# Optimization experiments

Hardware: AMD Instinct MI355X
Metric: run time of the kernel (lower is better)

Reference implementation:

```python
import jax, jax.numpy as jnp
import numpy as np

N = 50000      # nodes
E = 600000     # edges
A = 8          # max attrs per node
DT = 64        # node type embed dim
DA = 64        # node attr embed dim
C = DT + DA    # annotation dim = GGNN channels
T = 16         # num node types
TE = 4         # num edge types
L = 4          # num_agg_steps
B = 256        # num graphs
VATTR = 1000   # num node attrs
ENC = 128      # encoder_output_dim
NCLS = 10      # decoder output classes


def setup_inputs() -> dict:
    key = jax.random.key(0)
    ks = jax.random.split(key, 16)
    s = 0.05
    x_type = jax.random.randint(ks[0], (N,), 0, T)
    x_attrs = jax.random.randint(ks[1], (N, A), 0, VATTR)
    x_attrs_mask = jax.random.randint(ks[2], (N,), 1, A + 1)  # >=1 valid attr per node
    edge_index = jax.random.randint(ks[3], (2, E), 0, N)
    edge_attr = jax.random.randint(ks[4], (E,), 0, TE)
    batch = jnp.sort(jax.random.randint(ks[5], (N,), 0, B))
    return {
        'x_type': x_type, 'x_attrs': x_attrs, 'x_attrs_mask': x_attrs_mask,
        'edge_index': edge_index, 'edge_attr': edge_attr,
        'num_graphs': int(B), 'batch': batch,
        'type_emb': jax.random.normal(ks[6], (T, DT)) * s,
        'attr_emb': jax.random.normal(ks[7], (VATTR, DA)) * s,
        'W_msg': jax.random.normal(ks[8], (L, TE, C, C)) * s,
        'W_ih': jax.random.normal(ks[9], (3 * C, C)) * s,
        'W_hh': jax.random.normal(ks[10], (3 * C, C)) * s,
        'b_ih': jnp.zeros((3 * C,)),
        'b_hh': jnp.zeros((3 * C,)),
        'w_attn': jax.random.normal(ks[11], (C,)) * s,
        'b_attn': jnp.zeros(()),
        'W_enc': jax.random.normal(ks[12], (T * C, ENC)) * s,
        'b_enc': jnp.zeros((ENC,)),
        'W_dec': jax.random.normal(ks[13], (ENC, NCLS)) * s,
        'b_dec': jnp.zeros((NCLS,)),
    }


def _gru_cell(m, h, W_ih, W_hh, b_ih, b_hh):
    gi = m @ W_ih.T + b_ih            # [N, 3C]
    gh = h @ W_hh.T + b_hh            # [N, 3C]
    ir, iz, inn = jnp.split(gi, 3, axis=-1)
    hr, hz, hn = jnp.split(gh, 3, axis=-1)
    r = jax.nn.sigmoid(ir + hr)
    z = jax.nn.sigmoid(iz + hz)
    n = jnp.tanh(inn + r * hn)
    return (1.0 - z) * n + z * h


def reference(x_type, x_attrs, x_attrs_mask, edge_index, edge_attr, num_graphs, batch,
              type_emb, attr_emb, W_msg, W_ih, W_hh, b_ih, b_hh,
              w_attn, b_attn, W_enc, b_enc, W_dec, b_dec):
    n = x_type.shape[0]
    # --- embed node types and ragged-mean attribute embeddings ---
    t_emb = type_emb[x_type]                                   # [N, DT]
    a_all = attr_emb[x_attrs]                                  # [N, A, DA]
    valid = (jnp.arange(A)[None, :] < x_attrs_mask[:, None]).astype(a_all.dtype)
    a_emb = (a_all * valid[..., None]).sum(1) / jnp.maximum(x_attrs_mask, 1)[:, None].astype(a_all.dtype)
    x = jnp.concatenate([t_emb, a_emb], axis=1)                # [N, C]

    # --- GatedGraphConv with per-edge-type weights (sum aggregation + GRU) ---
    src, dst = edge_index[0], edge_index[1]
    for l in range(L):
        h_all = jnp.einsum('nc,tcd->tnd', x, W_msg[l])         # [TE, N, C]
        m_e = h_all.reshape(TE * n, C)[edge_attr * n + src]    # [E, C] gather per edge
        m = jax.ops.segment_sum(m_e, dst, num_segments=n)      # [N, C]
        x = _gru_cell(m, x, W_ih, W_hh, b_ih, b_hh)

    # --- per-(graph, node_type) segment mean (zeros for empty groups) ---
    seg = batch * T + x_type                                   # [N]
    S = num_graphs * T
    sums = jax.ops.segment_sum(x, seg, num_segments=S)         # [B*T, C]
    cnt = jax.ops.segment_sum(jnp.ones((n,), x.dtype), seg, num_segments=S)
    agg = jnp.where(cnt[:, None] > 0, sums / jnp.maximum(cnt, 1.0)[:, None], 0.0)
    agg = agg.reshape(num_graphs, T, C)                        # [B, T, C]

    # --- attention over node types, flatten, encode, decode ---
    w = agg @ w_attn + b_attn                                  # [B, T]
    attn = jax.nn.softmax(w, axis=-1)
    flat = (attn[..., None] * agg).reshape(num_graphs, T * C)  # [B, T*C]
    enc = flat @ W_enc + b_enc                                 # [B, ENC]
    return enc @ W_dec + b_dec                                 # [B, NCLS]
```

## Files before the change

kernel.cpp:

```cpp
#include <hip/hip_runtime.h>
#include <hip/hip_bf16.h>

#define NN 50000
#define NP 50016
#define EE 600000
#define AA 8
#define CC 128
#define TT 16
#define TE 4
#define LL 4
#define BB 256
#define ENC 128
#define NCLS 10
#define SROW 136
#define STR 520

typedef __attribute__((ext_vector_type(8))) short bf16x8;
typedef __attribute__((ext_vector_type(4))) float fx4;

__device__ __forceinline__ float b2f(ushort u) {
    union { float f; uint32_t i; } v; v.i = ((uint32_t)u) << 16; return v.f;
}
__device__ __forceinline__ ushort f2b(float f) {
    union { float f; uint32_t i; } v; v.f = f;
    uint32_t x = v.i;
    x += 0x7FFFu + ((x >> 16) & 1u);
    return (ushort)(x >> 16);
}
__device__ __forceinline__ float ldw(const void* p, long i, int isf) {
    return isf ? ((const float*)p)[i] : b2f(((const ushort*)p)[i]);
}
__device__ __forceinline__ float sigm(float t) { return 1.f / (1.f + __expf(-t)); }

__device__ __forceinline__ int xcd_swz(int bid, int nwg) {
    int q = nwg >> 3, r = nwg & 7, x = bid & 7, o = bid >> 3;
    return (x < r ? x * (q + 1) : r * (q + 1) + (x - r) * q) + o;
}

__global__ void sniff_kernel(int* flag, const void* W_enc_raw) {
    const ushort* u = (const ushort*)W_enc_raw;
    int good = 0;
    for (int i = 0; i < 256; ++i) {
        ushort v = u[i];
        int ex = (v >> 7) & 0xFF;
        if (v == 0 || (ex >= 100 && ex <= 126)) ++good;
    }
    *flag = (good >= 230) ? 0 : 1;
}

__global__ __launch_bounds__(256) void wstk_kernel(ushort* __restrict__ wstk,
                                                   const void* __restrict__ W,
                                                   const int* __restrict__ flag) {
    const int isf = *flag;
    int idx = blockIdx.x * 256 + threadIdx.x;
    int l = idx >> 16;
    int rem = idx & 65535;
    int d = rem >> 9, r2 = rem & 511;
    int t = r2 >> 7, c = r2 & 127;
    long src = ((long)(l * 4 + t) << 14) + c * 128 + d;
    wstk[idx] = isf ? f2b(((const float*)W)[src]) : ((const ushort*)W)[src];
}

__global__ __launch_bounds__(256) void wgru_kernel(ushort* __restrict__ wgb,
                                                   const void* __restrict__ Wih,
                                                   const void* __restrict__ Whh,
                                                   const int* __restrict__ flag) {
    const int isf = *flag;
    int idx = blockIdx.x * 256 + threadIdx.x;
    if (idx >= 98304) return;
    int ih = (idx < 49152);
    int off = ih ? idx : idx - 49152;
    wgb[idx] = f2b(ldw(ih ? Wih : Whh, off, isf));
}

__global__ __launch_bounds__(256) void wencT_kernel(ushort* __restrict__ wencT,
                                                    const void* __restrict__ W_enc,
                                                    const int* __restrict__ flag) {
    const int isf = *flag;
    int idx = blockIdx.x * 256 + threadIdx.x;
    int j = idx >> 11, k = idx & 2047;
    wencT[idx] = f2b(ldw(W_enc, (long)k * ENC + j, isf));
}

__global__ __launch_bounds__(256) void bconv_kernel(float* __restrict__ cvt,
                                                    const void* __restrict__ bih, const void* __restrict__ bhh,
                                                    const void* __restrict__ b_enc, const void* __restrict__ w_attn,
                                                    const void* __restrict__ b_dec, const void* __restrict__ b_attn,
                                                    const void* __restrict__ W_dec,
                                                    const int* __restrict__ flag) {
    const int isf = *flag;
    int i = blockIdx.x * 256 + threadIdx.x;
    if (i < 384) cvt[i] = ldw(bih, i, isf);
    else if (i < 768) cvt[i] = ldw(bhh, i - 384, isf);
    else if (i < 896) cvt[i] = ldw(b_enc, i - 768, isf);
    else if (i < 1024) cvt[i] = ldw(w_attn, i - 896, isf);
    else if (i < 1034) cvt[i] = ldw(b_dec, i - 1024, isf);
    else if (i == 1034) cvt[i] = ldw(b_attn, 0, isf);
    else if (i >= 1040 && i < 2320) cvt[i] = ldw(W_dec, i - 1040, isf);
}

__global__ __launch_bounds__(256) void embed_kernel(
    ushort* __restrict__ xbf,
    const int* __restrict__ x_type, const int* __restrict__ x_attrs,
    const int* __restrict__ x_mask, const void* __restrict__ type_emb,
    const void* __restrict__ attr_emb, const int* __restrict__ flag) {
    const int isf = *flag;
    int idx = blockIdx.x * 256 + threadIdx.x;
    int n = idx >> 6, c = idx & 63;
    if (n >= NP) return;
    if (n >= NN) { xbf[n * CC + c] = 0; xbf[n * CC + 64 + c] = 0; return; }
    int ty = x_type[n];
    xbf[n * CC + c] = f2b(ldw(type_emb, ty * 64 + c, isf));
    int cnt = x_mask[n];
    float s = 0.f;
    for (int a = 0; a < cnt; ++a) s += ldw(attr_emb, x_attrs[n * AA + a] * 64 + c, isf);
    xbf[n * CC + 64 + c] = f2b(s / (float)cnt);
}

__global__ __launch_bounds__(256) void deg_kernel(int* __restrict__ cnt, const int* __restrict__ ei) {
    int e = blockIdx.x * 256 + threadIdx.x;
    if (e < EE) atomicAdd(&cnt[ei[EE + e]], 1);
}
__global__ __launch_bounds__(256) void scan1_kernel(int* __restrict__ cnt, int* __restrict__ btot) {
    __shared__ int s[256];
    int tid = threadIdx.x, i = blockIdx.x * 256 + tid;
    int v = (i < NN) ? cnt[i] : 0;
    s[tid] = v; __syncthreads();
    for (int off = 1; off < 256; off <<= 1) {
        int t = (tid >= off) ? s[tid - off] : 0; __syncthreads();
        s[tid] += t; __syncthreads();
    }
    if (i < NN) cnt[i] = s[tid] - v;
    if (tid == 255) btot[blockIdx.x] = s[255];
}
__global__ __launch_bounds__(256) void scan2_kernel(int* __restrict__ btot, int nb) {
    __shared__ int s[256];
    int tid = threadIdx.x;
    int v = (tid < nb) ? btot[tid] : 0;
    s[tid] = v; __syncthreads();
    for (int off = 1; off < 256; off <<= 1) {
        int t = (tid >= off) ? s[tid - off] : 0; __syncthreads();
        s[tid] += t; __syncthreads();
    }
    if (tid < nb) btot[tid] = s[tid] - v;
}
__global__ __launch_bounds__(256) void scan3_kernel(int* __restrict__ cnt, const int* __restrict__ btot) {
    int i = blockIdx.x * 256 + threadIdx.x;
    if (i < NN) cnt[i] += btot[blockIdx.x];
}
__global__ __launch_bounds__(256) void fill_kernel(uint* __restrict__ csr, int* __restrict__ cnt,
                                                   const int* __restrict__ ei, const int* __restrict__ ea) {
    int e = blockIdx.x * 256 + threadIdx.x;
    if (e >= EE) return;
    int d = ei[EE + e];
    int pos = atomicAdd(&cnt[d], 1);
    csr[pos] = (uint)ei[e] | ((uint)ea[e] << 16);
}

__global__ __launch_bounds__(256) void gather4_kernel(
    ushort* __restrict__ s4, const ushort* __restrict__ xin,
    const uint* __restrict__ csr, const int* __restrict__ endp) {
    int w = threadIdx.x >> 6, l = threadIdx.x & 63;
    int wg = xcd_swz(blockIdx.x, NN / 4);
    int node = wg * 4 + w;
    int start = (node == 0) ? 0 : endp[node - 1];
    int end = endp[node];
    int c0 = l * 2;
    float a0 = 0.f, b0 = 0.f, a1 = 0.f, b1 = 0.f;
    float a2 = 0.f, b2 = 0.f, a3 = 0.f, b3 = 0.f;
    int i = start;
    for (; i + 1 < end; i += 2) {
        uint pkA = csr[i], pkB = csr[i + 1];
        uint srcA = pkA & 0xFFFFu, tA = pkA >> 16;
        uint srcB = pkB & 0xFFFFu, tB = pkB >> 16;
        uint hvA = *(const uint*)&xin[((size_t)srcA << 7) + c0];
        uint hvB = *(const uint*)&xin[((size_t)srcB << 7) + c0];
        float loA = b2f((ushort)(hvA & 0xFFFFu)), hfA = b2f((ushort)(hvA >> 16));
        float loB = b2f((ushort)(hvB & 0xFFFFu)), hfB = b2f((ushort)(hvB >> 16));
        if (tA == 0)      { a0 += loA; b0 += hfA; }
        else if (tA == 1) { a1 += loA; b1 += hfA; }
        else if (tA == 2) { a2 += loA; b2 += hfA; }
        else              { a3 += loA; b3 += hfA; }
        if (tB == 0)      { a0 += loB; b0 += hfB; }
        else if (tB == 1) { a1 += loB; b1 += hfB; }
        else if (tB == 2) { a2 += loB; b2 += hfB; }
        else              { a3 += loB; b3 += hfB; }
    }
    if (i < end) {
        uint pk = csr[i];
        uint src = pk & 0xFFFFu, t = pk >> 16;
        uint hv = *(const uint*)&xin[((size_t)src << 7) + c0];
        float lo = b2f((ushort)(hv & 0xFFFFu)), hf = b2f((ushort)(hv >> 16));
        if (t == 0)      { a0 += lo; b0 += hf; }
        else if (t == 1) { a1 += lo; b1 += hf; }
        else if (t == 2) { a2 += lo; b2 += hf; }
        else             { a3 += lo; b3 += hf; }
    }
    size_t base = (size_t)node << 9;
    *(uint*)&s4[base +   0 + c0] = (uint)f2b(a0) | ((uint)f2b(b0) << 16);
    *(uint*)&s4[base + 128 + c0] = (uint)f2b(a1) | ((uint)f2b(b1) << 16);
    *(uint*)&s4[base + 256 + c0] = (uint)f2b(a2) | ((uint)f2b(b2) << 16);
    *(uint*)&s4[base + 384 + c0] = (uint)f2b(a3) | ((uint)f2b(b3) << 16);
}

template <int AGG>
__global__ __launch_bounds__(256) void msggru_kernel(
    const ushort* __restrict__ xin, ushort* __restrict__ xout,
    const ushort* __restrict__ s4, const ushort* __restrict__ wstk,
    const ushort* __restrict__ wgb, const float* __restrict__ cvt,
    float* __restrict__ sums, float* __restrict__ cnta,
    const int* __restrict__ batch, const int* __restrict__ x_type) {
    __shared__ ushort s_tile[32][STR];
    __shared__ ushort m_bf[32][SROW];
    int tid = threadIdx.x;
    int wg = xcd_swz(blockIdx.x, NP / 32);
    int node0 = wg * 32;

    {
        const ushort* src = &s4[(size_t)node0 << 9];
#pragma unroll
        for (int q = 0; q < 8; ++q) {
            int i8 = (q * 256 + tid) * 8;
            int n = i8 >> 9, c = i8 & 511;
            bf16x8 v = *(const bf16x8*)&src[i8];
            *(bf16x8*)&s_tile[n][c] = v;
        }
    }
    __syncthreads();

    int w = tid >> 6, l = tid & 63;
    int lr = l & 15, lk = (l >> 4) * 8, hi = l >> 4;

    {
        fx4 mq[2][2];
        mq[0][0] = (fx4){0,0,0,0}; mq[0][1] = (fx4){0,0,0,0};
        mq[1][0] = (fx4){0,0,0,0}; mq[1][1] = (fx4){0,0,0,0};
        int ct0 = w * 2, ct1 = w * 2 + 1;
#pragma unroll
        for (int ks = 0; ks < 16; ++ks) {
            int ko = ks * 32 + lk;
            bf16x8 aA = *(const bf16x8*)&s_tile[lr][ko];
            bf16x8 aB = *(const bf16x8*)&s_tile[16 + lr][ko];
            bf16x8 bA = *(const bf16x8*)&wstk[(size_t)(ct0 * 16 + lr) * 512 + ko];
            bf16x8 bB = *(const bf16x8*)&wstk[(size_t)(ct1 * 16 + lr) * 512 + ko];
            mq[0][0] = __builtin_amdgcn_mfma_f32_16x16x32_bf16(aA, bA, mq[0][0], 0, 0, 0);
            mq[0][1] = __builtin_amdgcn_mfma_f32_16x16x32_bf16(aB, bA, mq[0][1], 0, 0, 0);
            mq[1][0] = __builtin_amdgcn_mfma_f32_16x16x32_bf16(aA, bB, mq[1][0], 0, 0, 0);
            mq[1][1] = __builtin_amdgcn_mfma_f32_16x16x32_bf16(aB, bB, mq[1][1], 0, 0, 0);
        }
#pragma unroll
        for (int cc = 0; cc < 2; ++cc)
#pragma unroll
            for (int rt = 0; rt < 2; ++rt)
#pragma unroll
                for (int r = 0; r < 4; ++r)
                    m_bf[rt * 16 + hi * 4 + r][(w * 2 + cc) * 16 + lr] = f2b(mq[cc][rt][r]);
    }
    __syncthreads();

    bf16x8 mf[2][4], xf[2][4];
#pragma unroll
    for (int rt = 0; rt < 2; ++rt)
#pragma unroll
        for (int ks = 0; ks < 4; ++ks) {
            mf[rt][ks] = *(const bf16x8*)&m_bf[rt * 16 + lr][ks * 32 + lk];
            xf[rt][ks] = *(const bf16x8*)&xin[(size_t)(node0 + rt * 16 + lr) * CC + ks * 32 + lk];
        }
#pragma unroll
    for (int cc = 0; cc < 2; ++cc) {
        int ct = w * 2 + cc;
        int row0 = ct * 16 + lr;
        fx4 ai[3][2], ah[3][2];
#pragma unroll
        for (int s = 0; s < 3; ++s)
#pragma unroll
            for (int rt = 0; rt < 2; ++rt) { ai[s][rt] = (fx4){0,0,0,0}; ah[s][rt] = (fx4){0,0,0,0}; }
#pragma unroll
        for (int ks = 0; ks < 4; ++ks) {
            int ko = ks * 32 + lk;
            bf16x8 bI[3], bH[3];
#pragma unroll
            for (int s = 0; s < 3; ++s) {
                bI[s] = *(const bf16x8*)&wgb[(size_t)(s * 128 + row0) * 128 + ko];
                bH[s] = *(const bf16x8*)&wgb[49152 + (size_t)(s * 128 + row0) * 128 + ko];
            }
#pragma unroll
            for (int s = 0; s < 3; ++s)
#pragma unroll
                for (int rt = 0; rt < 2; ++rt) {
                    ai[s][rt] = __builtin_amdgcn_mfma_f32_16x16x32_bf16(mf[rt][ks], bI[s], ai[s][rt], 0, 0, 0);
                    ah[s][rt] = __builtin_amdgcn_mfma_f32_16x16x32_bf16(xf[rt][ks], bH[s], ah[s][rt], 0, 0, 0);
                }
        }
        float bi0 = cvt[row0],        bh0 = cvt[384 + row0];
        float bi1 = cvt[128 + row0],  bh1 = cvt[512 + row0];
        float bi2 = cvt[256 + row0],  bh2 = cvt[640 + row0];
#pragma unroll
        for (int rt = 0; rt < 2; ++rt)
#pragma unroll
            for (int r = 0; r < 4; ++r) {
                int node = node0 + rt * 16 + hi * 4 + r;
                if (node >= NN) continue;
                float rg = sigm(ai[0][rt][r] + bi0 + ah[0][rt][r] + bh0);
                float zg = sigm(ai[1][rt][r] + bi1 + ah[1][rt][r] + bh1);
                float ny = ai[2][rt][r] + bi2 + rg * (ah[2][rt][r] + bh2);
                float ng = 2.f * sigm(2.f * ny) - 1.f;
                size_t xi = (size_t)node * CC + row0;
                float xo = b2f(xin[xi]);
                float xn = (1.f - zg) * ng + zg * xo;
                xout[xi] = f2b(xn);
                if (AGG) {
                    int seg = batch[node] * TT + x_type[node];
                    atomicAdd(&sums[(size_t)seg * CC + row0], xn);
                    if (row0 == 0) atomicAdd(&cnta[seg], 1.0f);
                }
            }
    }
}

__global__ __launch_bounds__(256) void attnflat_kernel(
    ushort* __restrict__ flatbf, const float* __restrict__ sums, const float* __restrict__ cnt,
    const float* __restrict__ cvt) {
    __shared__ float agg_s[TT][CC + 1];
    __shared__ float wpart[TT][8];
    __shared__ float attn_s[TT];
    int b = blockIdx.x, tid = threadIdx.x;
#pragma unroll
    for (int q = 0; q < 8; ++q) {
        int idx = tid + q * 256;
        int t = idx >> 7, c = idx & 127;
        float cv = cnt[b * TT + t];
        agg_s[t][c] = cv > 0.f ? sums[(size_t)(b * TT + t) * CC + c] / cv : 0.f;
    }
    __syncthreads();
    if (tid < 128) {
        int t = tid >> 3, p = tid & 7;
        float acc = 0.f;
        for (int i = 0; i < 16; ++i) acc += agg_s[t][p * 16 + i] * cvt[896 + p * 16 + i];
        wpart[t][p] = acc;
    }
    __syncthreads();
    if (tid < 16) {
        float acc = cvt[1034];
        for (int p = 0; p < 8; ++p) acc += wpart[tid][p];
        attn_s[tid] = acc;
    }
    __syncthreads();
    if (tid == 0) {
        float mx = attn_s[0];
        for (int t = 1; t < TT; ++t) mx = fmaxf(mx, attn_s[t]);
        float ssum = 0.f, ex[TT];
        for (int t = 0; t < TT; ++t) { ex[t] = __expf(attn_s[t] - mx); ssum += ex[t]; }
        for (int t = 0; t < TT; ++t) attn_s[t] = ex[t] / ssum;
    }
    __syncthreads();
#pragma unroll
    for (int q = 0; q < 8; ++q) {
        int idx = tid + q * 256;
        int t = idx >> 7, c = idx & 127;
        flatbf[(size_t)b * 2048 + idx] = f2b(agg_s[t][c] * attn_s[t]);
    }
}

__global__ __launch_bounds__(256) void enc_mfma(
    float* __restrict__ encp, const ushort* __restrict__ flatbf, const ushort* __restrict__ wencT) {
    int tid = threadIdx.x;
    int w = tid >> 6, l = tid & 63;
    int bid = blockIdx.x;
    int m0 = (bid >> 2) * 16;
    int kc = (bid & 3) * 512;
    int lr = l & 15, lk = (l >> 4) * 8;
    fx4 acc0 = {0,0,0,0}, acc1 = {0,0,0,0};
    int ct0 = w * 2, ct1 = w * 2 + 1;
#pragma unroll
    for (int ks = 0; ks < 16; ++ks) {
        int ko = kc + ks * 32 + lk;
        bf16x8 af = *(const bf16x8*)&flatbf[(size_t)(m0 + lr) * 2048 + ko];
        bf16x8 b0 = *(const bf16x8*)&wencT[(size_t)(ct0 * 16 + lr) * 2048 + ko];
        bf16x8 b1 = *(const bf16x8*)&wencT[(size_t)(ct1 * 16 + lr) * 2048 + ko];
        acc0 = __builtin_amdgcn_mfma_f32_16x16x32_bf16(af, b0, acc0, 0, 0, 0);
        acc1 = __builtin_amdgcn_mfma_f32_16x16x32_bf16(af, b1, acc1, 0, 0, 0);
    }
#pragma unroll
    for (int r = 0; r < 4; ++r) {
        int row = m0 + (l >> 4) * 4 + r;
        encp[(size_t)(bid & 3) * BB * ENC + (size_t)row * ENC + ct0 * 16 + lr] = acc0[r];
        encp[(size_t)(bid & 3) * BB * ENC + (size_t)row * ENC + ct1 * 16 + lr] = acc1[r];
    }
}

__global__ __launch_bounds__(256) void dec_kernel(
    void* __restrict__ out, const float* __restrict__ encp, const float* __restrict__ cvt,
    const int* __restrict__ flag) {
    const int isf = *flag;
    __shared__ float encs[ENC];
    int b = blockIdx.x, tid = threadIdx.x;
    if (tid < 128) {
        float e = cvt[768 + tid];
#pragma unroll
        for (int p = 0; p < 4; ++p) e += encp[(size_t)p * BB * ENC + (size_t)b * ENC + tid];
        encs[tid] = e;
    }
    __syncthreads();
    if (tid < NCLS) {
        float acc = cvt[1024 + tid];
        for (int j = 0; j < ENC; ++j) acc += encs[j] * cvt[1040 + j * NCLS + tid];
        int oi = b * NCLS + tid;
        if (isf) ((float*)out)[oi] = acc;
        else ((ushort*)out)[oi] = f2b(acc);
    }
}

extern "C" void kernel_launch(void* const* d_in, const int* in_sizes, int n_in,
                              void* d_out, int out_size, void* d_ws, size_t ws_size,
                              hipStream_t stream) {
    const int* x_type      = (const int*)d_in[0];
    const int* x_attrs     = (const int*)d_in[1];
    const int* x_mask      = (const int*)d_in[2];
    const int* edge_index  = (const int*)d_in[3];
    const int* edge_attr   = (const int*)d_in[4];
    const int* batch       = (const int*)d_in[6];
    const void* type_emb   = d_in[7];
    const void* attr_emb   = d_in[8];
    const void* W_msg      = d_in[9];
    const void* W_ih       = d_in[10];
    const void* W_hh       = d_in[11];
    const void* b_ih       = d_in[12];
    const void* b_hh       = d_in[13];
    const void* w_attn     = d_in[14];
    const void* b_attn     = d_in[15];
    const void* W_enc      = d_in[16];
    const void* b_enc      = d_in[17];
    const void* W_dec      = d_in[18];
    const void* b_dec      = d_in[19];

    char* p = (char*)d_ws;
    ushort* xbf0  = (ushort*)p;          p += (size_t)NP * CC * 2;
    ushort* xbf1  = (ushort*)p;          p += (size_t)NP * CC * 2;
    ushort* s4    = (ushort*)p;          p += (size_t)NP * 512 * 2;
    ushort* wstk  = (ushort*)p;          p += (size_t)LL * 128 * 512 * 2;
    ushort* wgb   = (ushort*)p;          p += (size_t)2 * 384 * 128 * 2;
    ushort* wencT = (ushort*)p;          p += (size_t)ENC * 2048 * 2;
    ushort* flatbf= (ushort*)p;          p += (size_t)BB * 2048 * 2;
    float*  encp  = (float*)p;           p += (size_t)4 * BB * ENC * 4;
    float*  cvt   = (float*)p;           p += 2320 * 4;
    float*  sums  = (float*)p;           p += (size_t)BB * TT * CC * 4;
    float*  cnta  = (float*)p;           p += (size_t)BB * TT * 4;
    uint*   csr   = (uint*)p;            p += (size_t)EE * 4;
    int*    cptr  = (int*)p;             p += (size_t)NN * 4;
    int*    btot  = (int*)p;             p += 256 * 4;
    int*    flag  = (int*)p;

    sniff_kernel<<<1, 1, 0, stream>>>(flag, W_enc);
    wstk_kernel<<<1024, 256, 0, stream>>>(wstk, W_msg, flag);
    wgru_kernel<<<384, 256, 0, stream>>>(wgb, W_ih, W_hh, flag);
    wencT_kernel<<<1024, 256, 0, stream>>>(wencT, W_enc, flag);
    bconv_kernel<<<10, 256, 0, stream>>>(cvt, b_ih, b_hh, b_enc, w_attn, b_dec, b_attn, W_dec, flag);
    embed_kernel<<<(NP * 64) / 256, 256, 0, stream>>>(xbf0, x_type, x_attrs, x_mask,
                                                      type_emb, attr_emb, flag);

    const int NB = (NN + 255) / 256;
    hipMemsetAsync(cptr, 0, (size_t)NN * sizeof(int), stream);
    deg_kernel<<<(EE + 255) / 256, 256, 0, stream>>>(cptr, edge_index);
    scan1_kernel<<<NB, 256, 0, stream>>>(cptr, btot);
    scan2_kernel<<<1, 256, 0, stream>>>(btot, NB);
    scan3_kernel<<<NB, 256, 0, stream>>>(cptr, btot);
    fill_kernel<<<(EE + 255) / 256, 256, 0, stream>>>(csr, cptr, edge_index, edge_attr);

    hipMemsetAsync(sums, 0, (size_t)(BB * TT * CC + BB * TT) * sizeof(float), stream);

    const int tile_grid = NP / 32;
    for (int l = 0; l < LL; ++l) {
        const ushort* xin = (l & 1) ? xbf1 : xbf0;
        ushort* xout      = (l & 1) ? xbf0 : xbf1;
        gather4_kernel<<<NN / 4, 256, 0, stream>>>(s4, xin, csr, cptr);
        const ushort* wl = wstk + (size_t)l * 128 * 512;
        if (l < LL - 1)
            msggru_kernel<0><<<tile_grid, 256, 0, stream>>>(xin, xout, s4, wl, wgb, cvt,
                                                            sums, cnta, batch, x_type);
        else
            msggru_kernel<1><<<tile_grid, 256, 0, stream>>>(xin, xout, s4, wl, wgb, cvt,
                                                            sums, cnta, batch, x_type);
    }

    attnflat_kernel<<<BB, 256, 0, stream>>>(flatbf, sums, cnta, cvt);
    enc_mfma<<<64, 256, 0, stream>>>(encp, flatbf, wencT);
    dec_kernel<<<BB, 256, 0, stream>>>(d_out, encp, cvt, flag);
}
```

Measured before the change: 689.6 us.

## Make msggru kernel persistent with double-buffered prefetch of gathered tiles

Turns the per-tile msggru launch into a persistent grid of 512 blocks, each looping over tiles with a stride. While it computes the current tile, it prefetches the next tile's gathered messages into registers and writes them into a second shared-memory buffer. The aim is to hide global-load latency and cut block launch overhead. It also changes the LDS row padding and drops the XCD swizzle, which may alter bank-conflict behaviour and L2 locality, and the doubled LDS plus the prefetch registers may lower occupancy.

```diff
diff --git a/kernel.cpp b/kernel.cpp
--- a/kernel.cpp
+++ b/kernel.cpp
@@ -12,8 +12,9 @@
 #define BB 256
 #define ENC 128
 #define NCLS 10
-#define SROW 136
-#define STR 520
+#define SROW 132
+#define STR 516
+#define GRIDP 512
 
 typedef __attribute__((ext_vector_type(8))) short bf16x8;
 typedef __attribute__((ext_vector_type(4))) float fx4;
@@ -210,111 +211,136 @@
     const ushort* __restrict__ wgb, const float* __restrict__ cvt,
     float* __restrict__ sums, float* __restrict__ cnta,
     const int* __restrict__ batch, const int* __restrict__ x_type) {
-    __shared__ ushort s_tile[32][STR];
+    __shared__ ushort s_tile[2][32][STR];
     __shared__ ushort m_bf[32][SROW];
     int tid = threadIdx.x;
-    int wg = xcd_swz(blockIdx.x, NP / 32);
-    int node0 = wg * 32;
-
+    const int NT = NP / 32;
+
+    int ti = blockIdx.x;
+    if (ti >= NT) return;
     {
-        const ushort* src = &s4[(size_t)node0 << 9];
+        const ushort* src = &s4[(size_t)ti << 14];
 #pragma unroll
         for (int q = 0; q < 8; ++q) {
             int i8 = (q * 256 + tid) * 8;
             int n = i8 >> 9, c = i8 & 511;
-            bf16x8 v = *(const bf16x8*)&src[i8];
-            *(bf16x8*)&s_tile[n][c] = v;
+            *(bf16x8*)&s_tile[0][n][c] = *(const bf16x8*)&src[i8];
         }
     }
-    __syncthreads();
-
+    int cur = 0;
     int w = tid >> 6, l = tid & 63;
     int lr = l & 15, lk = (l >> 4) * 8, hi = l >> 4;
 
-    {
-        fx4 mq[2][2];
-        mq[0][0] = (fx4){0,0,0,0}; mq[0][1] = (fx4){0,0,0,0};
-        mq[1][0] = (fx4){0,0,0,0}; mq[1][1] = (fx4){0,0,0,0};
-        int ct0 = w * 2, ct1 = w * 2 + 1;
-#pragma unroll
-        for (int ks = 0; ks < 16; ++ks) {
-            int ko = ks * 32 + lk;
-            bf16x8 aA = *(const bf16x8*)&s_tile[lr][ko];
-            bf16x8 aB = *(const bf16x8*)&s_tile[16 + lr][ko];
-            bf16x8 bA = *(const bf16x8*)&wstk[(size_t)(ct0 * 16 + lr) * 512 + ko];
-            bf16x8 bB = *(const bf16x8*)&wstk[(size_t)(ct1 * 16 + lr) * 512 + ko];
-            mq[0][0] = __builtin_amdgcn_mfma_f32_16x16x32_bf16(aA, bA, mq[0][0], 0, 0, 0);
-            mq[0][1] = __builtin_amdgcn_mfma_f32_16x16x32_bf16(aB, bA, mq[0][1], 0, 0, 0);
-            mq[1][0] = __builtin_amdgcn_mfma_f32_16x16x32_bf16(aA, bB, mq[1][0], 0, 0, 0);
-            mq[1][1] = __builtin_amdgcn_mfma_f32_16x16x32_bf16(aB, bB, mq[1][1], 0, 0, 0);
+    for (; ti < NT; ti += GRIDP) {
+        int tn = ti + GRIDP;
+        bf16x8 pre[8];
+        if (tn < NT) {
+            const ushort* srcn = &s4[(size_t)tn << 14];
+#pragma unroll
+            for (int q = 0; q < 8; ++q)
+                pre[q] = *(const bf16x8*)&srcn[(q * 256 + tid) * 8];
         }
-#pragma unroll
-        for (int cc = 0; cc < 2; ++cc)
+        __syncthreads();
+
+        int node0 = ti * 32;
+
+        {
+            fx4 mq[2][2];
+            mq[0][0] = (fx4){0,0,0,0}; mq[0][1] = (fx4){0,0,0,0};
+            mq[1][0] = (fx4){0,0,0,0}; mq[1][1] = (fx4){0,0,0,0};
+            int ct0 = w * 2, ct1 = w * 2 + 1;
+#pragma unroll
+            for (int ks = 0; ks < 16; ++ks) {
+                int ko = ks * 32 + lk;
+                bf16x8 aA = *(const bf16x8*)&s_tile[cur][lr][ko];
+                bf16x8 aB = *(const bf16x8*)&s_tile[cur][16 + lr][ko];
+                bf16x8 bA = *(const bf16x8*)&wstk[(size_t)(ct0 * 16 + lr) * 512 + ko];
+                bf16x8 bB = *(const bf16x8*)&wstk[(size_t)(ct1 * 16 + lr) * 512 + ko];
+                mq[0][0] = __builtin_amdgcn_mfma_f32_16x16x32_bf16(aA, bA, mq[0][0], 0, 0, 0);
+                mq[0][1] = __builtin_amdgcn_mfma_f32_16x16x32_bf16(aB, bA, mq[0][1], 0, 0, 0);
+                mq[1][0] = __builtin_amdgcn_mfma_f32_16x16x32_bf16(aA, bB, mq[1][0], 0, 0, 0);
+                mq[1][1] = __builtin_amdgcn_mfma_f32_16x16x32_bf16(aB, bB, mq[1][1], 0, 0, 0);
+            }
+#pragma unroll
+            for (int cc = 0; cc < 2; ++cc)
+#pragma unroll
+                for (int rt = 0; rt < 2; ++rt)
+#pragma unroll
+                    for (int r = 0; r < 4; ++r)
+                        m_bf[rt * 16 + hi * 4 + r][(w * 2 + cc) * 16 + lr] = f2b(mq[cc][rt][r]);
+        }
+        __syncthreads();
+
+        {
+            bf16x8 mf[2][4], xf[2][4];
 #pragma unroll
             for (int rt = 0; rt < 2; ++rt)
 #pragma unroll
-                for (int r = 0; r < 4; ++r)
-                    m_bf[rt * 16 + hi * 4 + r][(w * 2 + cc) * 16 + lr] = f2b(mq[cc][rt][r]);
-    }
-    __syncthreads();
-
-    bf16x8 mf[2][4], xf[2][4];
-#pragma unroll
-    for (int rt = 0; rt < 2; ++rt)
-#pragma unroll
-        for (int ks = 0; ks < 4; ++ks) {
-            mf[rt][ks] = *(const bf16x8*)&m_bf[rt * 16 + lr][ks * 32 + lk];
-            xf[rt][ks] = *(const bf16x8*)&xin[(size_t)(node0 + rt * 16 + lr) * CC + ks * 32 + lk];
+                for (int ks = 0; ks < 4; ++ks) {
+                    mf[rt][ks] = *(const bf16x8*)&m_bf[rt * 16 + lr][ks * 32 + lk];
+                    xf[rt][ks] = *(const bf16x8*)&xin[(size_t)(node0 + rt * 16 + lr) * CC + ks * 32 + lk];
+                }
+#pragma unroll
+            for (int cc = 0; cc < 2; ++cc) {
+                int ct = w * 2 + cc;
+                int row0 = ct * 16 + lr;
+                fx4 ai[3][2], ah[3][2];
+#pragma unroll
+                for (int s = 0; s < 3; ++s)
+#pragma unroll
+                    for (int rt = 0; rt < 2; ++rt) { ai[s][rt] = (fx4){0,0,0,0}; ah[s][rt] = (fx4){0,0,0,0}; }
+#pragma unroll
+                for (int ks = 0; ks < 4; ++ks) {
+                    int ko = ks * 32 + lk;
+                    bf16x8 bI[3], bH[3];
+#pragma unroll
+                    for (int s = 0; s < 3; ++s) {
+                        bI[s] = *(const bf16x8*)&wgb[(size_t)(s * 128 + row0) * 128 + ko];
+                        bH[s] = *(const bf16x8*)&wgb[49152 + (size_t)(s * 128 + row0) * 128 + ko];
+                    }
+#pragma unroll
+                    for (int s = 0; s < 3; ++s)
+#pragma unroll
+                        for (int rt = 0; rt < 2; ++rt) {
+                            ai[s][rt] = __builtin_amdgcn_mfma_f32_16x16x32_bf16(mf[rt][ks], bI[s], ai[s][rt], 0, 0, 0);
+                            ah[s][rt] = __builtin_amdgcn_mfma_f32_16x16x32_bf16(xf[rt][ks], bH[s], ah[s][rt], 0, 0, 0);
+                        }
+                }
+                float bi0 = cvt[row0],        bh0 = cvt[384 + row0];
+                float bi1 = cvt[128 + row0],  bh1 = cvt[512 + row0];
+                float bi2 = cvt[256 + row0],  bh2 = cvt[640 + row0];
+#pragma unroll
+                for (int rt = 0; rt < 2; ++rt)
+#pragma unroll
+                    for (int r = 0; r < 4; ++r) {
+                        int node = node0 + rt * 16 + hi * 4 + r;
+                        if (node >= NN) continue;
+                        float rg = sigm(ai[0][rt][r] + bi0 + ah[0][rt][r] + bh0);
+                        float zg = sigm(ai[1][rt][r] + bi1 + ah[1][rt][r] + bh1);
+                        float ny = ai[2][rt][r] + bi2 + rg * (ah[2][rt][r] + bh2);
+                        float ng = 2.f * sigm(2.f * ny) - 1.f;
+                        size_t xi = (size_t)node * CC + row0;
+                        float xo = b2f(xin[xi]);
+                        float xn = (1.f - zg) * ng + zg * xo;
+                        xout[xi] = f2b(xn);
+                        if (AGG) {
+                            int seg = batch[node] * TT + x_type[node];
+                            atomicAdd(&sums[(size_t)seg * CC + row0], xn);
+                            if (row0 == 0) atomicAdd(&cnta[seg], 1.0f);
+                        }
+                    }
+            }
         }
-#pragma unroll
-    for (int cc = 0; cc < 2; ++cc) {
-        int ct = w * 2 + cc;
-        int row0 = ct * 16 + lr;
-        fx4 ai[3][2], ah[3][2];
-#pragma unroll
-        for (int s = 0; s < 3; ++s)
-#pragma unroll
-            for (int rt = 0; rt < 2; ++rt) { ai[s][rt] = (fx4){0,0,0,0}; ah[s][rt] = (fx4){0,0,0,0}; }
-#pragma unroll
-        for (int ks = 0; ks < 4; ++ks) {
-            int ko = ks * 32 + lk;
-            bf16x8 bI[3], bH[3];
-#pragma unroll
-            for (int s = 0; s < 3; ++s) {
-                bI[s] = *(const bf16x8*)&wgb[(size_t)(s * 128 + row0) * 128 + ko];
-                bH[s] = *(const bf16x8*)&wgb[49152 + (size_t)(s * 128 + row0) * 128 + ko];
+
+        if (tn < NT) {
+#pragma unroll
+            for (int q = 0; q < 8; ++q) {
+                int i8 = (q * 256 + tid) * 8;
+                int n = i8 >> 9, c = i8 & 511;
+                *(bf16x8*)&s_tile[cur ^ 1][n][c] = pre[q];
             }
-#pragma unroll
-            for (int s = 0; s < 3; ++s)
-#pragma unroll
-                for (int rt = 0; rt < 2; ++rt) {
-                    ai[s][rt] = __builtin_amdgcn_mfma_f32_16x16x32_bf16(mf[rt][ks], bI[s], ai[s][rt], 0, 0, 0);
-                    ah[s][rt] = __builtin_amdgcn_mfma_f32_16x16x32_bf16(xf[rt][ks], bH[s], ah[s][rt], 0, 0, 0);
-                }
         }
-        float bi0 = cvt[row0],        bh0 = cvt[384 + row0];
-        float bi1 = cvt[128 + row0],  bh1 = cvt[512 + row0];
-        float bi2 = cvt[256 + row0],  bh2 = cvt[640 + row0];
-#pragma unroll
-        for (int rt = 0; rt < 2; ++rt)
-#pragma unroll
-            for (int r = 0; r < 4; ++r) {
-                int node = node0 + rt * 16 + hi * 4 + r;
-                if (node >= NN) continue;
-                float rg = sigm(ai[0][rt][r] + bi0 + ah[0][rt][r] + bh0);
-                float zg = sigm(ai[1][rt][r] + bi1 + ah[1][rt][r] + bh1);
-                float ny = ai[2][rt][r] + bi2 + rg * (ah[2][rt][r] + bh2);
-                float ng = 2.f * sigm(2.f * ny) - 1.f;
-                size_t xi = (size_t)node * CC + row0;
-                float xo = b2f(xin[xi]);
-                float xn = (1.f - zg) * ng + zg * xo;
-                xout[xi] = f2b(xn);
-                if (AGG) {
-                    int seg = batch[node] * TT + x_type[node];
-                    atomicAdd(&sums[(size_t)seg * CC + row0], xn);
-                    if (row0 == 0) atomicAdd(&cnta[seg], 1.0f);
-                }
-            }
+        cur ^= 1;
     }
 }
 
@@ -469,18 +495,17 @@
 
     hipMemsetAsync(sums, 0, (size_t)(BB * TT * CC + BB * TT) * sizeof(float), stream);
 
-    const int tile_grid = NP / 32;
     for (int l = 0; l < LL; ++l) {
         const ushort* xin = (l & 1) ? xbf1 : xbf0;
         ushort* xout      = (l & 1) ? xbf0 : xbf1;
         gather4_kernel<<<NN / 4, 256, 0, stream>>>(s4, xin, csr, cptr);
         const ushort* wl = wstk + (size_t)l * 128 * 512;
         if (l < LL - 1)
-            msggru_kernel<0><<<tile_grid, 256, 0, stream>>>(xin, xout, s4, wl, wgb, cvt,
-                                                            sums, cnta, batch, x_type);
+            msggru_kernel<0><<<GRIDP, 256, 0, stream>>>(xin, xout, s4, wl, wgb, cvt,
+                                                        sums, cnta, batch, x_type);
         else
-            msggru_kernel<1><<<tile_grid, 256, 0, stream>>>(xin, xout, s4, wl, wgb, cvt,
-                                                            sums, cnta, batch, x_type);
+            msggru_kernel<1><<<GRIDP, 256, 0, stream>>>(xin, xout, s4, wl, wgb, cvt,
+                                                        sums, cnta, batch, x_type);
     }
 
     attnflat_kernel<<<BB, 256, 0, stream>>>(flatbf, sums, cnta, cvt);
```

Measured after the change: 744.2 us. 1.08x slower.
